# Kernel tuning notes

Hardware: AMD Instinct MI355X
Metric: run time of the kernel (lower is better)

## Reference

```python
import jax, jax.numpy as jnp
import numpy as np

N_NODES = 50000
N_EDGES = 800000
IN_SIZE = 1024
EMB = 500


def setup_inputs() -> dict:
    key = jax.random.key(0)
    ks = jax.random.split(key, 9)
    x = jax.random.uniform(ks[0], (N_NODES, IN_SIZE), dtype=jnp.float32)
    edge_index = jax.random.randint(ks[1], (2, N_EDGES), 0, N_NODES, dtype=jnp.int32)
    edge_weight = jax.random.uniform(ks[2], (N_EDGES,), dtype=jnp.float32)
    s = 0.05
    wenc = jax.random.normal(ks[3], (EMB, IN_SIZE), dtype=jnp.float32) * s
    benc = jax.random.normal(ks[4], (EMB,), dtype=jnp.float32) * s
    wdec = jax.random.normal(ks[5], (IN_SIZE, EMB), dtype=jnp.float32) * s
    bdec = jax.random.normal(ks[6], (IN_SIZE,), dtype=jnp.float32) * s
    conv_weight = jax.random.normal(ks[7], (EMB, EMB), dtype=jnp.float32) * 0.1
    # lin.weight initialized N(0,0.1) + identity, per reset_parameters
    lin_weight = jax.random.normal(ks[8], (EMB, EMB), dtype=jnp.float32) * 0.1 + jnp.eye(EMB, dtype=jnp.float32)
    return {"x": x, "edge_index": edge_index, "edge_weight": edge_weight,
            "wenc": wenc, "benc": benc, "wdec": wdec, "bdec": bdec,
            "conv_weight": conv_weight, "lin_weight": lin_weight}


def reference(x, edge_index, edge_weight, wenc, benc, wdec, bdec, conv_weight, lin_weight):
    # encoder: h = sigmoid(x @ wenc^T + benc)          [N, EMB]
    h = jax.nn.sigmoid(x @ wenc.T + benc)
    # GraphConv (old PyG): neighbor transform then scatter-add to destinations
    h2 = h @ conv_weight                                # [N, EMB]
    src, dst = edge_index[0], edge_index[1]
    msgs = h2[src] * edge_weight[:, None]               # [E, EMB] gather + weight
    agg = jax.ops.segment_sum(msgs, dst, num_segments=x.shape[0])
    hout = agg + h @ lin_weight.T                       # root term via nn.Linear
    # decoder
    p = hout @ wdec.T + bdec                            # [N, IN_SIZE]
    return p
```

## Files before the change

### kernel.cpp

```cpp
#include <hip/hip_runtime.h>
#include <hip/hip_bf16.h>

typedef unsigned int u32;
typedef short bf16x8 __attribute__((ext_vector_type(8)));
typedef float floatx4 __attribute__((ext_vector_type(4)));

#define NNODES 50000
#define NEDGES 800000
#define INSZ   1024
#define EMB    500
#define EMBP   512

__device__ __forceinline__ short f2bf(float f) {
    u32 u = __builtin_bit_cast(u32, f);
    u32 r = u + 0x7FFFu + ((u >> 16) & 1u);
    return (short)(r >> 16);
}
__device__ __forceinline__ float bf2f(short h) {
    u32 u = ((u32)(unsigned short)h) << 16;
    return __builtin_bit_cast(float, u);
}

#define GLDS16(gp, lp) __builtin_amdgcn_global_load_lds( \
    (const __attribute__((address_space(1))) u32*)(gp),  \
    (__attribute__((address_space(3))) u32*)(lp), 16, 0, 0)

__device__ __forceinline__ u32 xcd_swz(u32 orig, u32 q, u32 r) {
    u32 xcd = orig & 7u, seq = orig >> 3;
    u32 base = (xcd < r) ? xcd * (q + 1u) : r * (q + 1u) + (xcd - r) * q;
    return base + seq;
}

__global__ void pack_all(const float* __restrict__ wenc, const float* __restrict__ conv,
                         const float* __restrict__ lin,  const float* __restrict__ wdec,
                         short* __restrict__ wencP, short* __restrict__ wdecP,
                         short* __restrict__ Bw) {
    int tid = blockIdx.x * 256 + threadIdx.x;
    {
        int m = tid >> 10, k = tid & 1023;
        wencP[tid] = (m < EMB) ? f2bf(wenc[m * INSZ + k]) : (short)0;
    }
    {
        int m = tid >> 9, k = tid & 511;
        wdecP[tid] = (k < EMB) ? f2bf(wdec[m * EMB + k]) : (short)0;
    }
    {
        int kk = tid >> 9, j = tid & 511;
        short v = 0;
        if (j < EMB) {
            if (kk < EMB)                          v = f2bf(conv[kk * EMB + j]);
            else if (kk >= 512 && kk - 512 < EMB)  v = f2bf(lin[j * EMB + (kk - 512)]);
        }
        Bw[tid] = v;
    }
}

__global__ __launch_bounds__(256)
void conv_x(const float* __restrict__ X, short* __restrict__ Xb) {
    size_t base = ((size_t)blockIdx.x * 256 + threadIdx.x) * 8;
    floatx4 f0 = *(const floatx4*)(X + base);
    floatx4 f1 = *(const floatx4*)(X + base + 4);
    bf16x8 p;
#pragma unroll
    for (int j = 0; j < 4; ++j) { p[j] = f2bf(f0[j]); p[4 + j] = f2bf(f1[j]); }
    *(bf16x8*)(Xb + base) = p;
}


__global__ __launch_bounds__(256)
void gemm_wpre(const short* __restrict__ Ap, const short* __restrict__ Bp,
               short* __restrict__ Wbig) {
    __shared__ short As[2][128 * 32];
    __shared__ short Bs[2][128 * 32];
    const int tid  = threadIdx.x;
    const int lane = tid & 63;
    const int wave = tid >> 6;
    const int wr   = (wave >> 1) * 64;
    const int wc   = (wave & 1) * 64;
    const int rowBase = blockIdx.y * 128;
    const int colBase = blockIdx.x * 128;

    floatx4 acc[4][4] = {};

    const int r0 = tid >> 2;
    const int c0 = (tid & 3) * 8;
    const short* aP0 = Ap + (size_t)(rowBase + r0) * EMBP + c0;
    const short* aP1 = Ap + (size_t)(rowBase + r0 + 64) * EMBP + c0;
    const short* bP0 = Bp + (size_t)(colBase + r0) * EMBP + c0;
    const short* bP1 = Bp + (size_t)(colBase + r0 + 64) * EMBP + c0;

    const int q8  = (lane >> 4) * 8;
    const int m16 = lane & 15;

#define STAGE_W(buf, k0)                                   \
    GLDS16(aP0 + (k0), &As[buf][tid * 8]);                 \
    GLDS16(aP1 + (k0), &As[buf][2048 + tid * 8]);          \
    GLDS16(bP0 + (k0), &Bs[buf][tid * 8]);                 \
    GLDS16(bP1 + (k0), &Bs[buf][2048 + tid * 8]);

    STAGE_W(0, 0);
    __syncthreads();
    int cur = 0;
    for (int t = 0; t < 16; ++t) {
        if (t + 1 < 16) { STAGE_W(cur ^ 1, (t + 1) * 32); }
        bf16x8 af[4], bfr[4];
#pragma unroll
        for (int i = 0; i < 4; ++i) {
            af[i]  = *(const bf16x8*)&As[cur][(wr + i * 16 + m16) * 32 + q8];
            bfr[i] = *(const bf16x8*)&Bs[cur][(wc + i * 16 + m16) * 32 + q8];
        }
#pragma unroll
        for (int i = 0; i < 4; ++i)
#pragma unroll
            for (int j = 0; j < 4; ++j)
                acc[i][j] = __builtin_amdgcn_mfma_f32_16x16x32_bf16(af[i], bfr[j], acc[i][j], 0, 0, 0);
        __syncthreads();
        cur ^= 1;
    }
#undef STAGE_W

    const int rq = (lane >> 4) * 4;
#pragma unroll
    for (int i = 0; i < 4; ++i)
#pragma unroll
        for (int j = 0; j < 4; ++j)
#pragma unroll
            for (int reg = 0; reg < 4; ++reg) {
                int row = rowBase + wr + i * 16 + rq + reg;
                int col = colBase + wc + j * 16 + m16;
                Wbig[(size_t)row * 1024 + col] = f2bf(acc[i][j][reg]);
            }
}

__global__ __launch_bounds__(256)
void gemm_enc(const short* __restrict__ Xb, const short* __restrict__ Wp,
              const float* __restrict__ benc, short* __restrict__ H) {
    __shared__ short As[2][128 * 32];
    __shared__ short Bs[2][128 * 32];
    const int tid  = threadIdx.x;
    const int lane = tid & 63;
    const int wave = tid >> 6;
    const int wr   = (wave >> 1) * 64;
    const int wc   = (wave & 1) * 64;
    const u32 swz  = xcd_swz(blockIdx.y * 4 + blockIdx.x, 195, 4);
    const int rowBase = (int)(swz >> 2) * 128;
    const int colBase = (int)(swz & 3) * 128;

    floatx4 acc[4][4] = {};

    const int r0 = tid >> 2;
    const int c0 = (tid & 3) * 8;
    int ar0 = rowBase + r0;       if (ar0 >= NNODES) ar0 = NNODES - 1;
    int ar1 = rowBase + r0 + 64;  if (ar1 >= NNODES) ar1 = NNODES - 1;
    const short* aP0 = Xb + (size_t)ar0 * INSZ + c0;
    const short* aP1 = Xb + (size_t)ar1 * INSZ + c0;
    const short* bP0 = Wp + (size_t)(colBase + r0) * INSZ + c0;
    const short* bP1 = Wp + (size_t)(colBase + r0 + 64) * INSZ + c0;

    const int q8  = (lane >> 4) * 8;
    const int m16 = lane & 15;

#define STAGE_E(buf, k0)                                   \
    GLDS16(aP0 + (k0), &As[buf][tid * 8]);                 \
    GLDS16(aP1 + (k0), &As[buf][2048 + tid * 8]);          \
    GLDS16(bP0 + (k0), &Bs[buf][tid * 8]);                 \
    GLDS16(bP1 + (k0), &Bs[buf][2048 + tid * 8]);

    STAGE_E(0, 0);
    __syncthreads();
    int cur = 0;
    for (int t = 0; t < 32; ++t) {
        if (t + 1 < 32) { STAGE_E(cur ^ 1, (t + 1) * 32); }
        bf16x8 af[4], bfr[4];
#pragma unroll
        for (int i = 0; i < 4; ++i) {
            af[i]  = *(const bf16x8*)&As[cur][(wr + i * 16 + m16) * 32 + q8];
            bfr[i] = *(const bf16x8*)&Bs[cur][(wc + i * 16 + m16) * 32 + q8];
        }
#pragma unroll
        for (int i = 0; i < 4; ++i)
#pragma unroll
            for (int j = 0; j < 4; ++j)
                acc[i][j] = __builtin_amdgcn_mfma_f32_16x16x32_bf16(af[i], bfr[j], acc[i][j], 0, 0, 0);
        __syncthreads();
        cur ^= 1;
    }
#undef STAGE_E

    const int rq = (lane >> 4) * 4;
#pragma unroll
    for (int i = 0; i < 4; ++i)
#pragma unroll
        for (int j = 0; j < 4; ++j)
#pragma unroll
            for (int reg = 0; reg < 4; ++reg) {
                int row = rowBase + wr + i * 16 + rq + reg;
                int col = colBase + wc + j * 16 + m16;
                if (row < NNODES) {
                    float b = (col < EMB) ? benc[col] : 0.f;
                    float v = 1.f / (1.f + __expf(-(acc[i][j][reg] + b)));
                    H[(size_t)row * EMBP + col] = f2bf(v);
                }
            }
}

__global__ __launch_bounds__(256)
void gemm_fused(const short* __restrict__ AggB, const short* __restrict__ H,
                const short* __restrict__ Wb, const float* __restrict__ bdec,
                float* __restrict__ Out) {
    __shared__ short As[2][128 * 32];
    __shared__ short Bs[2][128 * 32];
    const int tid  = threadIdx.x;
    const int lane = tid & 63;
    const int wave = tid >> 6;
    const int wr   = (wave >> 1) * 64;
    const int wc   = (wave & 1) * 64;
    const u32 swz  = xcd_swz(blockIdx.y * 8 + blockIdx.x, 391, 0);
    const int rowBase = (int)(swz >> 3) * 128;
    const int colBase = (int)(swz & 7) * 128;

    floatx4 acc[4][4] = {};

    const int r0 = tid >> 2;
    const int c0 = (tid & 3) * 8;
    int ar0 = rowBase + r0;       if (ar0 >= NNODES) ar0 = NNODES - 1;
    int ar1 = rowBase + r0 + 64;  if (ar1 >= NNODES) ar1 = NNODES - 1;
    const short* agP0 = AggB + (size_t)ar0 * EMBP + c0;
    const short* agP1 = AggB + (size_t)ar1 * EMBP + c0;
    const short* hP0  = H + (size_t)ar0 * EMBP + c0;
    const short* hP1  = H + (size_t)ar1 * EMBP + c0;
    const short* wP0  = Wb + (size_t)(colBase + r0) * 1024 + c0;
    const short* wP1  = Wb + (size_t)(colBase + r0 + 64) * 1024 + c0;

    const int q8  = (lane >> 4) * 8;
    const int m16 = lane & 15;

#define STAGE_F(buf, k0)                                              \
    if ((k0) < 512) {                                                 \
        GLDS16(agP0 + (k0), &As[buf][tid * 8]);                       \
        GLDS16(agP1 + (k0), &As[buf][2048 + tid * 8]);                \
    } else {                                                          \
        GLDS16(hP0 + ((k0) - 512), &As[buf][tid * 8]);                \
        GLDS16(hP1 + ((k0) - 512), &As[buf][2048 + tid * 8]);         \
    }                                                                 \
    GLDS16(wP0 + (k0), &Bs[buf][tid * 8]);                            \
    GLDS16(wP1 + (k0), &Bs[buf][2048 + tid * 8]);

    STAGE_F(0, 0);
    __syncthreads();
    int cur = 0;
    for (int t = 0; t < 32; ++t) {
        if (t + 1 < 32) { STAGE_F(cur ^ 1, (t + 1) * 32); }
        bf16x8 af[4], bfr[4];
#pragma unroll
        for (int i = 0; i < 4; ++i) {
            af[i]  = *(const bf16x8*)&As[cur][(wr + i * 16 + m16) * 32 + q8];
            bfr[i] = *(const bf16x8*)&Bs[cur][(wc + i * 16 + m16) * 32 + q8];
        }
#pragma unroll
        for (int i = 0; i < 4; ++i)
#pragma unroll
            for (int j = 0; j < 4; ++j)
                acc[i][j] = __builtin_amdgcn_mfma_f32_16x16x32_bf16(af[i], bfr[j], acc[i][j], 0, 0, 0);
        __syncthreads();
        cur ^= 1;
    }
#undef STAGE_F

    const int rq = (lane >> 4) * 4;
#pragma unroll
    for (int i = 0; i < 4; ++i)
#pragma unroll
        for (int j = 0; j < 4; ++j)
#pragma unroll
            for (int reg = 0; reg < 4; ++reg) {
                int row = rowBase + wr + i * 16 + rq + reg;
                int col = colBase + wc + j * 16 + m16;
                if (row < NNODES)
                    Out[(size_t)row * INSZ + col] = acc[i][j][reg] + bdec[col];
            }
}

__global__ __launch_bounds__(256)
void count_edges(const int* __restrict__ dst, int* __restrict__ counts) {
    int e = blockIdx.x * 256 + threadIdx.x;
    atomicAdd(&counts[dst[e]], 1);
}

__global__ __launch_bounds__(1024)
void scan_counts(const int* __restrict__ counts, int* __restrict__ rowPtr,
                 int* __restrict__ cursor) {
    __shared__ int wsum[16];
    __shared__ int sbase;
    const int t = threadIdx.x;
    const int lane = t & 63;
    const int wv = t >> 6;
    if (t == 0) sbase = 0;
    for (int chunk = 0; chunk < 50176; chunk += 1024) {
        int i = chunk + t;
        int c = (i < NNODES) ? counts[i] : 0;
        int v = c;
#pragma unroll
        for (int off = 1; off < 64; off <<= 1) {
            int u = __shfl_up(v, off, 64);
            if (lane >= off) v += u;
        }
        if (lane == 63) wsum[wv] = v;
        __syncthreads();
        int woff = 0, total = 0;
#pragma unroll
        for (int w = 0; w < 16; ++w) {
            int s = wsum[w];
            if (w < wv) woff += s;
            total += s;
        }
        int base = sbase;
        __syncthreads();
        if (i < NNODES) {
            int p = base + woff + v - c;
            rowPtr[i] = p;
            cursor[i] = p;
        }
        if (t == 0) sbase = base + total;
        __syncthreads();
    }
}

__global__ __launch_bounds__(256)
void fill_csr(const int* __restrict__ src, const int* __restrict__ dst,
              const float* __restrict__ ew, int* __restrict__ cursor,
              int* __restrict__ csrSrc, float* __restrict__ csrW) {
    int e = blockIdx.x * 256 + threadIdx.x;
    int d = dst[e];
    int p = atomicAdd(&cursor[d], 1);
    csrSrc[p] = src[e];
    csrW[p]   = ew[e];
}

__global__ __launch_bounds__(256)
void aggregate(const short* __restrict__ H, const int* __restrict__ rowPtr,
               const int* __restrict__ counts, const int* __restrict__ csrSrc,
               const float* __restrict__ csrW, short* __restrict__ aggB) {
    const int n    = blockIdx.x * 4 + (threadIdx.x >> 6);
    const int lane = threadIdx.x & 63;
    const int beg  = rowPtr[n];
    const int cnt  = counts[n];
    const short* hb = H + lane * 8;

    float acc[8] = {0.f, 0.f, 0.f, 0.f, 0.f, 0.f, 0.f, 0.f};
    int i = 0;
    for (; i + 8 <= cnt; i += 8) {
        int   s[8]; float w[8]; bf16x8 v[8];
#pragma unroll
        for (int u = 0; u < 8; ++u) { s[u] = csrSrc[beg + i + u]; w[u] = csrW[beg + i + u]; }
#pragma unroll
        for (int u = 0; u < 8; ++u) v[u] = *(const bf16x8*)(hb + (size_t)s[u] * EMBP);
#pragma unroll
        for (int u = 0; u < 8; ++u)
#pragma unroll
            for (int j = 0; j < 8; ++j)
                acc[j] += w[u] * bf2f(v[u][j]);
    }
    for (; i + 4 <= cnt; i += 4) {
        int   s[4]; float w[4]; bf16x8 v[4];
#pragma unroll
        for (int u = 0; u < 4; ++u) { s[u] = csrSrc[beg + i + u]; w[u] = csrW[beg + i + u]; }
#pragma unroll
        for (int u = 0; u < 4; ++u) v[u] = *(const bf16x8*)(hb + (size_t)s[u] * EMBP);
#pragma unroll
        for (int u = 0; u < 4; ++u)
#pragma unroll
            for (int j = 0; j < 8; ++j)
                acc[j] += w[u] * bf2f(v[u][j]);
    }
    for (; i < cnt; ++i) {
        int   s0 = csrSrc[beg + i];
        float w0 = csrW[beg + i];
        bf16x8 v0 = *(const bf16x8*)(hb + (size_t)s0 * EMBP);
#pragma unroll
        for (int j = 0; j < 8; ++j)
            acc[j] += w0 * bf2f(v0[j]);
    }

    bf16x8 o;
#pragma unroll
    for (int j = 0; j < 8; ++j) o[j] = f2bf(acc[j]);
    *(bf16x8*)(aggB + (size_t)n * EMBP + lane * 8) = o;
}

extern "C" void kernel_launch(void* const* d_in, const int* in_sizes, int n_in,
                              void* d_out, int out_size, void* d_ws, size_t ws_size,
                              hipStream_t stream) {
    const float* x    = (const float*)d_in[0];
    const int*   ei   = (const int*)d_in[1];
    const float* ew   = (const float*)d_in[2];
    const float* wenc = (const float*)d_in[3];
    const float* benc = (const float*)d_in[4];
    const float* wdec = (const float*)d_in[5];
    const float* bdec = (const float*)d_in[6];
    const float* conv = (const float*)d_in[7];
    const float* lin  = (const float*)d_in[8];
    float* out = (float*)d_out;

    char* ws = (char*)d_ws;
    short* wencP = (short*)(ws);
    short* wdecP = (short*)(ws + 1048576);
    short* Bw    = (short*)(ws + 2097152);
    short* Wbig  = (short*)(ws + 3145728);
    short* h     = (short*)(ws + 5242880);
    short* aggB  = (short*)(ws + 5242880 + 51200000);

    short* Xbf  = (short*)((char*)d_out + 102400000);
    char*  scratch = (char*)d_out + 102400000;
    int*   counts = (int*)scratch;
    int*   rowPtr = counts + NNODES;
    int*   cursor = rowPtr + NNODES;
    int*   csrSrc = cursor + NNODES;
    float* csrW   = (float*)(csrSrc + NEDGES);

    dim3 blk(256);
    pack_all<<<2048, blk, 0, stream>>>(wenc, conv, lin, wdec, wencP, wdecP, Bw);

    gemm_wpre<<<dim3(8, 8), blk, 0, stream>>>(wdecP, Bw, Wbig);

    conv_x<<<25000, blk, 0, stream>>>(x, Xbf);

    int rowTiles = (NNODES + 127) / 128;

    gemm_enc<<<dim3(EMBP / 128, rowTiles), blk, 0, stream>>>(Xbf, wencP, benc, h);

    hipMemsetAsync(counts, 0, (size_t)NNODES * 4, stream);
    count_edges<<<NEDGES / 256, blk, 0, stream>>>(ei + NEDGES, counts);
    scan_counts<<<1, 1024, 0, stream>>>(counts, rowPtr, cursor);
    fill_csr<<<NEDGES / 256, blk, 0, stream>>>(ei, ei + NEDGES, ew, cursor, csrSrc, csrW);
    aggregate<<<NNODES / 4, blk, 0, stream>>>(h, rowPtr, counts, csrSrc, csrW, aggB);

    gemm_fused<<<dim3(INSZ / 128, rowTiles), blk, 0, stream>>>(aggB, h, Wbig, bdec, out);
}
```

Baseline: 917.5 us.

## Fuse prep kernels, parallelize scan, and enlarge GEMM tiles to 256x256

Merges X conversion, weight packing and edge counting into one prep kernel, replaces the single-block serial scan with a 196-block scan where each block recomputes its prefix, and grows the encoder and decoder GEMM tiles to 256x256 with 512 threads and 8x4 MFMA accumulators per wave. CSR scratch moves to the start of the output buffer, and the aggregate 4-way tail loop is removed. The aim is to cut launch overhead, the serial scan latency, and global/LDS traffic per FLOP. The larger tiles raise register and LDS pressure, which may reduce occupancy, and the scan does redundant prefix summing.

```diff
diff --git a/kernel.cpp b/kernel.cpp
--- a/kernel.cpp
+++ b/kernel.cpp
@@ -31,41 +31,47 @@
     return base + seq;
 }
 
-__global__ void pack_all(const float* __restrict__ wenc, const float* __restrict__ conv,
-                         const float* __restrict__ lin,  const float* __restrict__ wdec,
-                         short* __restrict__ wencP, short* __restrict__ wdecP,
-                         short* __restrict__ Bw) {
-    int tid = blockIdx.x * 256 + threadIdx.x;
+__global__ __launch_bounds__(256)
+void prep(const float* __restrict__ X, const float* __restrict__ wenc,
+          const float* __restrict__ conv, const float* __restrict__ lin,
+          const float* __restrict__ wdec, const int* __restrict__ dst,
+          short* __restrict__ Xb, short* __restrict__ wencP,
+          short* __restrict__ wdecP, short* __restrict__ Bw,
+          int* __restrict__ counts) {
+    const int b = blockIdx.x;
+    const int gid = b * 256 + threadIdx.x;
     {
-        int m = tid >> 10, k = tid & 1023;
-        wencP[tid] = (m < EMB) ? f2bf(wenc[m * INSZ + k]) : (short)0;
-    }
-    {
-        int m = tid >> 9, k = tid & 511;
-        wdecP[tid] = (k < EMB) ? f2bf(wdec[m * EMB + k]) : (short)0;
-    }
-    {
-        int kk = tid >> 9, j = tid & 511;
-        short v = 0;
-        if (j < EMB) {
-            if (kk < EMB)                          v = f2bf(conv[kk * EMB + j]);
-            else if (kk >= 512 && kk - 512 < EMB)  v = f2bf(lin[j * EMB + (kk - 512)]);
+        size_t base = (size_t)gid * 8;
+        floatx4 f0 = *(const floatx4*)(X + base);
+        floatx4 f1 = *(const floatx4*)(X + base + 4);
+        bf16x8 p;
+#pragma unroll
+        for (int j = 0; j < 4; ++j) { p[j] = f2bf(f0[j]); p[4 + j] = f2bf(f1[j]); }
+        *(bf16x8*)(Xb + base) = p;
+    }
+    if (b < 2048) {
+        {
+            int m = gid >> 10, k = gid & 1023;
+            wencP[gid] = (m < EMB) ? f2bf(wenc[m * INSZ + k]) : (short)0;
         }
-        Bw[tid] = v;
-    }
-}
-
-__global__ __launch_bounds__(256)
-void conv_x(const float* __restrict__ X, short* __restrict__ Xb) {
-    size_t base = ((size_t)blockIdx.x * 256 + threadIdx.x) * 8;
-    floatx4 f0 = *(const floatx4*)(X + base);
-    floatx4 f1 = *(const floatx4*)(X + base + 4);
-    bf16x8 p;
-#pragma unroll
-    for (int j = 0; j < 4; ++j) { p[j] = f2bf(f0[j]); p[4 + j] = f2bf(f1[j]); }
-    *(bf16x8*)(Xb + base) = p;
-}
-
+        {
+            int m = gid >> 9, k = gid & 511;
+            wdecP[gid] = (k < EMB) ? f2bf(wdec[m * EMB + k]) : (short)0;
+        }
+        {
+            int kk = gid >> 9, j = gid & 511;
+            short v = 0;
+            if (j < EMB) {
+                if (kk < EMB)                          v = f2bf(conv[kk * EMB + j]);
+                else if (kk >= 512 && kk - 512 < EMB)  v = f2bf(lin[j * EMB + (kk - 512)]);
+            }
+            Bw[gid] = v;
+        }
+    }
+    if (b < 3125) {
+        atomicAdd(&counts[dst[gid]], 1);
+    }
+}
 
 __global__ __launch_bounds__(256)
 void gemm_wpre(const short* __restrict__ Ap, const short* __restrict__ Bp,
@@ -132,53 +138,55 @@
             }
 }
 
-__global__ __launch_bounds__(256)
+
+__global__ __launch_bounds__(512)
 void gemm_enc(const short* __restrict__ Xb, const short* __restrict__ Wp,
               const float* __restrict__ benc, short* __restrict__ H) {
-    __shared__ short As[2][128 * 32];
-    __shared__ short Bs[2][128 * 32];
+    __shared__ short As[2][256 * 32];
+    __shared__ short Bs[2][256 * 32];
     const int tid  = threadIdx.x;
     const int lane = tid & 63;
     const int wave = tid >> 6;
-    const int wr   = (wave >> 1) * 64;
-    const int wc   = (wave & 1) * 64;
-    const u32 swz  = xcd_swz(blockIdx.y * 4 + blockIdx.x, 195, 4);
-    const int rowBase = (int)(swz >> 2) * 128;
-    const int colBase = (int)(swz & 3) * 128;
-
-    floatx4 acc[4][4] = {};
+    const int wm   = wave >> 2;
+    const int wn   = wave & 3;
+    const u32 swz  = xcd_swz(blockIdx.x, 49, 0);
+    const int rowBase = (int)(swz >> 1) * 256;
+    const int colBase = (int)(swz & 1) * 256;
+
+    floatx4 acc[8][4] = {};
 
     const int r0 = tid >> 2;
     const int c0 = (tid & 3) * 8;
-    int ar0 = rowBase + r0;       if (ar0 >= NNODES) ar0 = NNODES - 1;
-    int ar1 = rowBase + r0 + 64;  if (ar1 >= NNODES) ar1 = NNODES - 1;
+    int ar0 = rowBase + r0;        if (ar0 >= NNODES) ar0 = NNODES - 1;
+    int ar1 = rowBase + r0 + 128;  if (ar1 >= NNODES) ar1 = NNODES - 1;
     const short* aP0 = Xb + (size_t)ar0 * INSZ + c0;
     const short* aP1 = Xb + (size_t)ar1 * INSZ + c0;
     const short* bP0 = Wp + (size_t)(colBase + r0) * INSZ + c0;
-    const short* bP1 = Wp + (size_t)(colBase + r0 + 64) * INSZ + c0;
+    const short* bP1 = Wp + (size_t)(colBase + r0 + 128) * INSZ + c0;
 
     const int q8  = (lane >> 4) * 8;
     const int m16 = lane & 15;
 
 #define STAGE_E(buf, k0)                                   \
     GLDS16(aP0 + (k0), &As[buf][tid * 8]);                 \
-    GLDS16(aP1 + (k0), &As[buf][2048 + tid * 8]);          \
+    GLDS16(aP1 + (k0), &As[buf][4096 + tid * 8]);          \
     GLDS16(bP0 + (k0), &Bs[buf][tid * 8]);                 \
-    GLDS16(bP1 + (k0), &Bs[buf][2048 + tid * 8]);
+    GLDS16(bP1 + (k0), &Bs[buf][4096 + tid * 8]);
 
     STAGE_E(0, 0);
     __syncthreads();
     int cur = 0;
     for (int t = 0; t < 32; ++t) {
         if (t + 1 < 32) { STAGE_E(cur ^ 1, (t + 1) * 32); }
-        bf16x8 af[4], bfr[4];
-#pragma unroll
-        for (int i = 0; i < 4; ++i) {
-            af[i]  = *(const bf16x8*)&As[cur][(wr + i * 16 + m16) * 32 + q8];
-            bfr[i] = *(const bf16x8*)&Bs[cur][(wc + i * 16 + m16) * 32 + q8];
-        }
-#pragma unroll
-        for (int i = 0; i < 4; ++i)
+        bf16x8 af[8], bfr[4];
+#pragma unroll
+        for (int i = 0; i < 8; ++i)
+            af[i]  = *(const bf16x8*)&As[cur][(wm * 128 + i * 16 + m16) * 32 + q8];
+#pragma unroll
+        for (int j = 0; j < 4; ++j)
+            bfr[j] = *(const bf16x8*)&Bs[cur][(wn * 64 + j * 16 + m16) * 32 + q8];
+#pragma unroll
+        for (int i = 0; i < 8; ++i)
 #pragma unroll
             for (int j = 0; j < 4; ++j)
                 acc[i][j] = __builtin_amdgcn_mfma_f32_16x16x32_bf16(af[i], bfr[j], acc[i][j], 0, 0, 0);
@@ -189,13 +197,13 @@
 
     const int rq = (lane >> 4) * 4;
 #pragma unroll
-    for (int i = 0; i < 4; ++i)
+    for (int i = 0; i < 8; ++i)
 #pragma unroll
         for (int j = 0; j < 4; ++j)
 #pragma unroll
             for (int reg = 0; reg < 4; ++reg) {
-                int row = rowBase + wr + i * 16 + rq + reg;
-                int col = colBase + wc + j * 16 + m16;
+                int row = rowBase + wm * 128 + i * 16 + rq + reg;
+                int col = colBase + wn * 64 + j * 16 + m16;
                 if (row < NNODES) {
                     float b = (col < EMB) ? benc[col] : 0.f;
                     float v = 1.f / (1.f + __expf(-(acc[i][j][reg] + b)));
@@ -204,33 +212,33 @@
             }
 }
 
-__global__ __launch_bounds__(256)
+__global__ __launch_bounds__(512)
 void gemm_fused(const short* __restrict__ AggB, const short* __restrict__ H,
                 const short* __restrict__ Wb, const float* __restrict__ bdec,
                 float* __restrict__ Out) {
-    __shared__ short As[2][128 * 32];
-    __shared__ short Bs[2][128 * 32];
+    __shared__ short As[2][256 * 32];
+    __shared__ short Bs[2][256 * 32];
     const int tid  = threadIdx.x;
     const int lane = tid & 63;
     const int wave = tid >> 6;
-    const int wr   = (wave >> 1) * 64;
-    const int wc   = (wave & 1) * 64;
-    const u32 swz  = xcd_swz(blockIdx.y * 8 + blockIdx.x, 391, 0);
-    const int rowBase = (int)(swz >> 3) * 128;
-    const int colBase = (int)(swz & 7) * 128;
-
-    floatx4 acc[4][4] = {};
+    const int wm   = wave >> 2;
+    const int wn   = wave & 3;
+    const u32 swz  = xcd_swz(blockIdx.x, 98, 0);
+    const int rowBase = (int)(swz >> 2) * 256;
+    const int colBase = (int)(swz & 3) * 256;
+
+    floatx4 acc[8][4] = {};
 
     const int r0 = tid >> 2;
     const int c0 = (tid & 3) * 8;
-    int ar0 = rowBase + r0;       if (ar0 >= NNODES) ar0 = NNODES - 1;
-    int ar1 = rowBase + r0 + 64;  if (ar1 >= NNODES) ar1 = NNODES - 1;
+    int ar0 = rowBase + r0;        if (ar0 >= NNODES) ar0 = NNODES - 1;
+    int ar1 = rowBase + r0 + 128;  if (ar1 >= NNODES) ar1 = NNODES - 1;
     const short* agP0 = AggB + (size_t)ar0 * EMBP + c0;
     const short* agP1 = AggB + (size_t)ar1 * EMBP + c0;
     const short* hP0  = H + (size_t)ar0 * EMBP + c0;
     const short* hP1  = H + (size_t)ar1 * EMBP + c0;
     const short* wP0  = Wb + (size_t)(colBase + r0) * 1024 + c0;
-    const short* wP1  = Wb + (size_t)(colBase + r0 + 64) * 1024 + c0;
+    const short* wP1  = Wb + (size_t)(colBase + r0 + 128) * 1024 + c0;
 
     const int q8  = (lane >> 4) * 8;
     const int m16 = lane & 15;
@@ -238,27 +246,28 @@
 #define STAGE_F(buf, k0)                                              \
     if ((k0) < 512) {                                                 \
         GLDS16(agP0 + (k0), &As[buf][tid * 8]);                       \
-        GLDS16(agP1 + (k0), &As[buf][2048 + tid * 8]);                \
+        GLDS16(agP1 + (k0), &As[buf][4096 + tid * 8]);                \
     } else {                                                          \
         GLDS16(hP0 + ((k0) - 512), &As[buf][tid * 8]);                \
-        GLDS16(hP1 + ((k0) - 512), &As[buf][2048 + tid * 8]);         \
+        GLDS16(hP1 + ((k0) - 512), &As[buf][4096 + tid * 8]);         \
     }                                                                 \
     GLDS16(wP0 + (k0), &Bs[buf][tid * 8]);                            \
-    GLDS16(wP1 + (k0), &Bs[buf][2048 + tid * 8]);
+    GLDS16(wP1 + (k0), &Bs[buf][4096 + tid * 8]);
 
     STAGE_F(0, 0);
     __syncthreads();
     int cur = 0;
     for (int t = 0; t < 32; ++t) {
         if (t + 1 < 32) { STAGE_F(cur ^ 1, (t + 1) * 32); }
-        bf16x8 af[4], bfr[4];
-#pragma unroll
-        for (int i = 0; i < 4; ++i) {
-            af[i]  = *(const bf16x8*)&As[cur][(wr + i * 16 + m16) * 32 + q8];
-            bfr[i] = *(const bf16x8*)&Bs[cur][(wc + i * 16 + m16) * 32 + q8];
-        }
-#pragma unroll
-        for (int i = 0; i < 4; ++i)
+        bf16x8 af[8], bfr[4];
+#pragma unroll
+        for (int i = 0; i < 8; ++i)
+            af[i]  = *(const bf16x8*)&As[cur][(wm * 128 + i * 16 + m16) * 32 + q8];
+#pragma unroll
+        for (int j = 0; j < 4; ++j)
+            bfr[j] = *(const bf16x8*)&Bs[cur][(wn * 64 + j * 16 + m16) * 32 + q8];
+#pragma unroll
+        for (int i = 0; i < 8; ++i)
 #pragma unroll
             for (int j = 0; j < 4; ++j)
                 acc[i][j] = __builtin_amdgcn_mfma_f32_16x16x32_bf16(af[i], bfr[j], acc[i][j], 0, 0, 0);
@@ -269,60 +278,52 @@
 
     const int rq = (lane >> 4) * 4;
 #pragma unroll
-    for (int i = 0; i < 4; ++i)
+    for (int i = 0; i < 8; ++i)
 #pragma unroll
         for (int j = 0; j < 4; ++j)
 #pragma unroll
             for (int reg = 0; reg < 4; ++reg) {
-                int row = rowBase + wr + i * 16 + rq + reg;
-                int col = colBase + wc + j * 16 + m16;
+                int row = rowBase + wm * 128 + i * 16 + rq + reg;
+                int col = colBase + wn * 64 + j * 16 + m16;
                 if (row < NNODES)
                     Out[(size_t)row * INSZ + col] = acc[i][j][reg] + bdec[col];
             }
 }
 
 __global__ __launch_bounds__(256)
-void count_edges(const int* __restrict__ dst, int* __restrict__ counts) {
-    int e = blockIdx.x * 256 + threadIdx.x;
-    atomicAdd(&counts[dst[e]], 1);
-}
-
-__global__ __launch_bounds__(1024)
 void scan_counts(const int* __restrict__ counts, int* __restrict__ rowPtr,
                  int* __restrict__ cursor) {
-    __shared__ int wsum[16];
-    __shared__ int sbase;
+    __shared__ int lsum[4];
+    __shared__ int wsc[4];
+    const int b = blockIdx.x;
     const int t = threadIdx.x;
     const int lane = t & 63;
     const int wv = t >> 6;
-    if (t == 0) sbase = 0;
-    for (int chunk = 0; chunk < 50176; chunk += 1024) {
-        int i = chunk + t;
-        int c = (i < NNODES) ? counts[i] : 0;
-        int v = c;
-#pragma unroll
-        for (int off = 1; off < 64; off <<= 1) {
-            int u = __shfl_up(v, off, 64);
-            if (lane >= off) v += u;
-        }
-        if (lane == 63) wsum[wv] = v;
-        __syncthreads();
-        int woff = 0, total = 0;
-#pragma unroll
-        for (int w = 0; w < 16; ++w) {
-            int s = wsum[w];
-            if (w < wv) woff += s;
-            total += s;
-        }
-        int base = sbase;
-        __syncthreads();
-        if (i < NNODES) {
-            int p = base + woff + v - c;
-            rowPtr[i] = p;
-            cursor[i] = p;
-        }
-        if (t == 0) sbase = base + total;
-        __syncthreads();
+
+    int pre = 0;
+    for (int i = t; i < b * 256; i += 256) pre += counts[i];
+#pragma unroll
+    for (int off = 1; off < 64; off <<= 1) pre += __shfl_xor(pre, off, 64);
+    if (lane == 0) lsum[wv] = pre;
+
+    int i = b * 256 + t;
+    int c = (i < NNODES) ? counts[i] : 0;
+    int v = c;
+#pragma unroll
+    for (int off = 1; off < 64; off <<= 1) {
+        int u = __shfl_up(v, off, 64);
+        if (lane >= off) v += u;
+    }
+    if (lane == 63) wsc[wv] = v;
+    __syncthreads();
+
+    int base = lsum[0] + lsum[1] + lsum[2] + lsum[3];
+    int woff = 0;
+    for (int w = 0; w < wv; ++w) woff += wsc[w];
+    if (i < NNODES) {
+        int p = base + woff + v - c;
+        rowPtr[i] = p;
+        cursor[i] = p;
     }
 }
 
@@ -357,18 +358,6 @@
         for (int u = 0; u < 8; ++u) v[u] = *(const bf16x8*)(hb + (size_t)s[u] * EMBP);
 #pragma unroll
         for (int u = 0; u < 8; ++u)
-#pragma unroll
-            for (int j = 0; j < 8; ++j)
-                acc[j] += w[u] * bf2f(v[u][j]);
-    }
-    for (; i + 4 <= cnt; i += 4) {
-        int   s[4]; float w[4]; bf16x8 v[4];
-#pragma unroll
-        for (int u = 0; u < 4; ++u) { s[u] = csrSrc[beg + i + u]; w[u] = csrW[beg + i + u]; }
-#pragma unroll
-        for (int u = 0; u < 4; ++u) v[u] = *(const bf16x8*)(hb + (size_t)s[u] * EMBP);
-#pragma unroll
-        for (int u = 0; u < 4; ++u)
 #pragma unroll
             for (int j = 0; j < 8; ++j)
                 acc[j] += w[u] * bf2f(v[u][j]);
@@ -410,30 +399,28 @@
     short* h     = (short*)(ws + 5242880);
     short* aggB  = (short*)(ws + 5242880 + 51200000);
 
-    short* Xbf  = (short*)((char*)d_out + 102400000);
-    char*  scratch = (char*)d_out + 102400000;
+    char*  scratch = (char*)d_out;
     int*   counts = (int*)scratch;
     int*   rowPtr = counts + NNODES;
     int*   cursor = rowPtr + NNODES;
     int*   csrSrc = cursor + NNODES;
     float* csrW   = (float*)(csrSrc + NEDGES);
+    short* Xbf    = (short*)((char*)d_out + 102400000);
 
     dim3 blk(256);
-    pack_all<<<2048, blk, 0, stream>>>(wenc, conv, lin, wdec, wencP, wdecP, Bw);
+    hipMemsetAsync(counts, 0, (size_t)NNODES * 4, stream);
+
+    prep<<<25000, blk, 0, stream>>>(x, wenc, conv, lin, wdec, ei + NEDGES,
+                                    Xbf, wencP, wdecP, Bw, counts);
 
     gemm_wpre<<<dim3(8, 8), blk, 0, stream>>>(wdecP, Bw, Wbig);
 
-    conv_x<<<25000, blk, 0, stream>>>(x, Xbf);
-
-    int rowTiles = (NNODES + 127) / 128;
-
-    gemm_enc<<<dim3(EMBP / 128, rowTiles), blk, 0, stream>>>(Xbf, wencP, benc, h);
-
-    hipMemsetAsync(counts, 0, (size_t)NNODES * 4, stream);
-    count_edges<<<NEDGES / 256, blk, 0, stream>>>(ei + NEDGES, counts);
-    scan_counts<<<1, 1024, 0, stream>>>(counts, rowPtr, cursor);
+    scan_counts<<<196, blk, 0, stream>>>(counts, rowPtr, cursor);
     fill_csr<<<NEDGES / 256, blk, 0, stream>>>(ei, ei + NEDGES, ew, cursor, csrSrc, csrW);
+
+    gemm_enc<<<392, dim3(512), 0, stream>>>(Xbf, wencP, benc, h);
+
     aggregate<<<NNODES / 4, blk, 0, stream>>>(h, rowPtr, counts, csrSrc, csrW, aggB);
 
-    gemm_fused<<<dim3(INSZ / 128, rowTiles), blk, 0, stream>>>(aggB, h, Wbig, bdec, out);
-}
+    gemm_fused<<<784, dim3(512), 0, stream>>>(aggB, h, Wbig, bdec, out);
+}
```

Result: no change. 919.4 us (+0.2%).

## Fuse prep kernels, parallelize count scan, and reorder CSR build before encoder

Applied to the files above, without the earlier changes.

Merges the weight packing, x-to-bf16 conversion and edge counting into one launch. It replaces the single-block serial scan with a 196-block scan in which each block recomputes its prefix by summing all earlier counts. The CSR scratch buffers move to the start of the output buffer and the CSR build is scheduled before the encoder GEMM. The aggregate kernel's 4-edge remainder loop is dropped, so leftover edges go through the scalar tail. The goal is fewer launches and no long single-block scan, at the cost of redundant prefix reads and a longer scalar tail.

```diff
diff --git a/kernel.cpp b/kernel.cpp
--- a/kernel.cpp
+++ b/kernel.cpp
@@ -31,41 +31,47 @@
     return base + seq;
 }
 
-__global__ void pack_all(const float* __restrict__ wenc, const float* __restrict__ conv,
-                         const float* __restrict__ lin,  const float* __restrict__ wdec,
-                         short* __restrict__ wencP, short* __restrict__ wdecP,
-                         short* __restrict__ Bw) {
-    int tid = blockIdx.x * 256 + threadIdx.x;
+__global__ __launch_bounds__(256)
+void prep(const float* __restrict__ X, const float* __restrict__ wenc,
+          const float* __restrict__ conv, const float* __restrict__ lin,
+          const float* __restrict__ wdec, const int* __restrict__ dst,
+          short* __restrict__ Xb, short* __restrict__ wencP,
+          short* __restrict__ wdecP, short* __restrict__ Bw,
+          int* __restrict__ counts) {
+    const int b = blockIdx.x;
+    const int gid = b * 256 + threadIdx.x;
     {
-        int m = tid >> 10, k = tid & 1023;
-        wencP[tid] = (m < EMB) ? f2bf(wenc[m * INSZ + k]) : (short)0;
-    }
-    {
-        int m = tid >> 9, k = tid & 511;
-        wdecP[tid] = (k < EMB) ? f2bf(wdec[m * EMB + k]) : (short)0;
-    }
-    {
-        int kk = tid >> 9, j = tid & 511;
-        short v = 0;
-        if (j < EMB) {
-            if (kk < EMB)                          v = f2bf(conv[kk * EMB + j]);
-            else if (kk >= 512 && kk - 512 < EMB)  v = f2bf(lin[j * EMB + (kk - 512)]);
-        }
-        Bw[tid] = v;
-    }
-}
-
-__global__ __launch_bounds__(256)
-void conv_x(const float* __restrict__ X, short* __restrict__ Xb) {
-    size_t base = ((size_t)blockIdx.x * 256 + threadIdx.x) * 8;
-    floatx4 f0 = *(const floatx4*)(X + base);
-    floatx4 f1 = *(const floatx4*)(X + base + 4);
-    bf16x8 p;
-#pragma unroll
-    for (int j = 0; j < 4; ++j) { p[j] = f2bf(f0[j]); p[4 + j] = f2bf(f1[j]); }
-    *(bf16x8*)(Xb + base) = p;
-}
-
+        size_t base = (size_t)gid * 8;
+        floatx4 f0 = *(const floatx4*)(X + base);
+        floatx4 f1 = *(const floatx4*)(X + base + 4);
+        bf16x8 p;
+#pragma unroll
+        for (int j = 0; j < 4; ++j) { p[j] = f2bf(f0[j]); p[4 + j] = f2bf(f1[j]); }
+        *(bf16x8*)(Xb + base) = p;
+    }
+    if (b < 2048) {
+        {
+            int m = gid >> 10, k = gid & 1023;
+            wencP[gid] = (m < EMB) ? f2bf(wenc[m * INSZ + k]) : (short)0;
+        }
+        {
+            int m = gid >> 9, k = gid & 511;
+            wdecP[gid] = (k < EMB) ? f2bf(wdec[m * EMB + k]) : (short)0;
+        }
+        {
+            int kk = gid >> 9, j = gid & 511;
+            short v = 0;
+            if (j < EMB) {
+                if (kk < EMB)                          v = f2bf(conv[kk * EMB + j]);
+                else if (kk >= 512 && kk - 512 < EMB)  v = f2bf(lin[j * EMB + (kk - 512)]);
+            }
+            Bw[gid] = v;
+        }
+    }
+    if (b < 3125) {
+        atomicAdd(&counts[dst[gid]], 1);
+    }
+}
 
 __global__ __launch_bounds__(256)
 void gemm_wpre(const short* __restrict__ Ap, const short* __restrict__ Bp,
@@ -131,6 +137,7 @@
                 Wbig[(size_t)row * 1024 + col] = f2bf(acc[i][j][reg]);
             }
 }
+
 
 __global__ __launch_bounds__(256)
 void gemm_enc(const short* __restrict__ Xb, const short* __restrict__ Wp,
@@ -282,47 +289,39 @@
 }
 
 __global__ __launch_bounds__(256)
-void count_edges(const int* __restrict__ dst, int* __restrict__ counts) {
-    int e = blockIdx.x * 256 + threadIdx.x;
-    atomicAdd(&counts[dst[e]], 1);
-}
-
-__global__ __launch_bounds__(1024)
 void scan_counts(const int* __restrict__ counts, int* __restrict__ rowPtr,
                  int* __restrict__ cursor) {
-    __shared__ int wsum[16];
-    __shared__ int sbase;
+    __shared__ int lsum[4];
+    __shared__ int wsc[4];
+    const int b = blockIdx.x;
     const int t = threadIdx.x;
     const int lane = t & 63;
     const int wv = t >> 6;
-    if (t == 0) sbase = 0;
-    for (int chunk = 0; chunk < 50176; chunk += 1024) {
-        int i = chunk + t;
-        int c = (i < NNODES) ? counts[i] : 0;
-        int v = c;
-#pragma unroll
-        for (int off = 1; off < 64; off <<= 1) {
-            int u = __shfl_up(v, off, 64);
-            if (lane >= off) v += u;
-        }
-        if (lane == 63) wsum[wv] = v;
-        __syncthreads();
-        int woff = 0, total = 0;
-#pragma unroll
-        for (int w = 0; w < 16; ++w) {
-            int s = wsum[w];
-            if (w < wv) woff += s;
-            total += s;
-        }
-        int base = sbase;
-        __syncthreads();
-        if (i < NNODES) {
-            int p = base + woff + v - c;
-            rowPtr[i] = p;
-            cursor[i] = p;
-        }
-        if (t == 0) sbase = base + total;
-        __syncthreads();
+
+    int pre = 0;
+    for (int i = t; i < b * 256; i += 256) pre += counts[i];
+#pragma unroll
+    for (int off = 1; off < 64; off <<= 1) pre += __shfl_xor(pre, off, 64);
+    if (lane == 0) lsum[wv] = pre;
+
+    int i = b * 256 + t;
+    int c = (i < NNODES) ? counts[i] : 0;
+    int v = c;
+#pragma unroll
+    for (int off = 1; off < 64; off <<= 1) {
+        int u = __shfl_up(v, off, 64);
+        if (lane >= off) v += u;
+    }
+    if (lane == 63) wsc[wv] = v;
+    __syncthreads();
+
+    int base = lsum[0] + lsum[1] + lsum[2] + lsum[3];
+    int woff = 0;
+    for (int w = 0; w < wv; ++w) woff += wsc[w];
+    if (i < NNODES) {
+        int p = base + woff + v - c;
+        rowPtr[i] = p;
+        cursor[i] = p;
     }
 }
 
@@ -357,18 +356,6 @@
         for (int u = 0; u < 8; ++u) v[u] = *(const bf16x8*)(hb + (size_t)s[u] * EMBP);
 #pragma unroll
         for (int u = 0; u < 8; ++u)
-#pragma unroll
-            for (int j = 0; j < 8; ++j)
-                acc[j] += w[u] * bf2f(v[u][j]);
-    }
-    for (; i + 4 <= cnt; i += 4) {
-        int   s[4]; float w[4]; bf16x8 v[4];
-#pragma unroll
-        for (int u = 0; u < 4; ++u) { s[u] = csrSrc[beg + i + u]; w[u] = csrW[beg + i + u]; }
-#pragma unroll
-        for (int u = 0; u < 4; ++u) v[u] = *(const bf16x8*)(hb + (size_t)s[u] * EMBP);
-#pragma unroll
-        for (int u = 0; u < 4; ++u)
 #pragma unroll
             for (int j = 0; j < 8; ++j)
                 acc[j] += w[u] * bf2f(v[u][j]);
@@ -410,30 +397,28 @@
     short* h     = (short*)(ws + 5242880);
     short* aggB  = (short*)(ws + 5242880 + 51200000);
 
-    short* Xbf  = (short*)((char*)d_out + 102400000);
-    char*  scratch = (char*)d_out + 102400000;
+    char*  scratch = (char*)d_out;
     int*   counts = (int*)scratch;
     int*   rowPtr = counts + NNODES;
     int*   cursor = rowPtr + NNODES;
     int*   csrSrc = cursor + NNODES;
     float* csrW   = (float*)(csrSrc + NEDGES);
+    short* Xbf    = (short*)((char*)d_out + 102400000);
 
     dim3 blk(256);
-    pack_all<<<2048, blk, 0, stream>>>(wenc, conv, lin, wdec, wencP, wdecP, Bw);
+    hipMemsetAsync(counts, 0, (size_t)NNODES * 4, stream);
+
+    prep<<<25000, blk, 0, stream>>>(x, wenc, conv, lin, wdec, ei + NEDGES,
+                                    Xbf, wencP, wdecP, Bw, counts);
 
     gemm_wpre<<<dim3(8, 8), blk, 0, stream>>>(wdecP, Bw, Wbig);
 
-    conv_x<<<25000, blk, 0, stream>>>(x, Xbf);
-
-    int rowTiles = (NNODES + 127) / 128;
-
-    gemm_enc<<<dim3(EMBP / 128, rowTiles), blk, 0, stream>>>(Xbf, wencP, benc, h);
-
-    hipMemsetAsync(counts, 0, (size_t)NNODES * 4, stream);
-    count_edges<<<NEDGES / 256, blk, 0, stream>>>(ei + NEDGES, counts);
-    scan_counts<<<1, 1024, 0, stream>>>(counts, rowPtr, cursor);
+    scan_counts<<<196, blk, 0, stream>>>(counts, rowPtr, cursor);
     fill_csr<<<NEDGES / 256, blk, 0, stream>>>(ei, ei + NEDGES, ew, cursor, csrSrc, csrW);
+
+    gemm_enc<<<dim3(EMBP / 128, (NNODES + 127) / 128), blk, 0, stream>>>(Xbf, wencP, benc, h);
+
     aggregate<<<NNODES / 4, blk, 0, stream>>>(h, rowPtr, counts, csrSrc, csrW, aggB);
 
-    gemm_fused<<<dim3(INSZ / 128, rowTiles), blk, 0, stream>>>(aggB, h, Wbig, bdec, out);
-}
+    gemm_fused<<<dim3(INSZ / 128, (NNODES + 127) / 128), blk, 0, stream>>>(aggB, h, Wbig, bdec, out);
+}
```

After: 878.4 us. 1.04x faster.
